# Optimization experiments

Measured on AMD Instinct MI355X. Metric: run time of the kernel, lower is better.

The kernel has to match this reference:

```python
import jax, jax.numpy as jnp
import numpy as np

EPS = 1e-4  # matches init_kwargs eps


def setup_inputs() -> dict:
    key = jax.random.key(0)
    k1, k2, k3 = jax.random.split(key, 3)
    B, C, T = 64, 256, 2048
    x = jax.random.normal(k1, (B, C, T), dtype=jnp.float32)
    # per-timestep BatchNorm affine params: [T, C]
    gamma = 1.0 + 0.1 * jax.random.normal(k2, (T, C), dtype=jnp.float32)
    beta = 0.01 * jax.random.normal(k3, (T, C), dtype=jnp.float32)
    return {"x": x, "gamma": gamma, "beta": beta}


def reference(x, gamma, beta):
    # BNTTv1 (training mode): every timestep's BatchNorm1d sees the FULL [B, C, T]
    # tensor, so the batch statistics (per-channel mean/var over B and T) are
    # identical across timesteps. Only the affine (gamma_t, beta_t) differs, and
    # the module keeps just slice t of layer t's output. Equivalent fused form:
    mean = jnp.mean(x, axis=(0, 2), keepdims=True)            # [1, C, 1]
    var = jnp.mean((x - mean) ** 2, axis=(0, 2), keepdims=True)  # biased var
    norm = (x - mean) * jax.lax.rsqrt(var + EPS)              # [B, C, T]
    # gamma/beta: [T, C] -> broadcast as [1, C, T]
    out = norm * gamma.T[None, :, :] + beta.T[None, :, :]
    return out
```

## Files before the change

kernel.cpp:

```cpp
#include <hip/hip_runtime.h>
#include <hip/hip_bf16.h>

#define B_ 64
#define C_ 256
#define T_ 2048
#define EPS_ 1e-4f
#define NPC ((float)(B_ * T_))

#define SPLITS 8
#define BPB (B_ / SPLITS)
#define T4 (T_ / 4)

typedef float f4 __attribute__((ext_vector_type(4)));

__global__ __launch_bounds__(256) void bntt_stats(const float* __restrict__ x,
                                                  float* __restrict__ partials) {
    const int c   = blockIdx.x & (C_ - 1);
    const int s   = blockIdx.x >> 8;
    const int tid = threadIdx.x;

    float sum = 0.0f, sumsq = 0.0f;
    const int b0 = s * BPB;
    #pragma unroll
    for (int b = 0; b < BPB; ++b) {
        const f4* p = (const f4*)(x + (size_t)(b0 + b) * (C_ * T_) + (size_t)c * T_);
        #pragma unroll
        for (int i = 0; i < T4 / 256; ++i) {
            f4 v = p[tid + i * 256];
            sum   += v.x + v.y + v.z + v.w;
            sumsq += v.x * v.x + v.y * v.y + v.z * v.z + v.w * v.w;
        }
    }
    #pragma unroll
    for (int off = 32; off > 0; off >>= 1) {
        sum   += __shfl_down(sum, off);
        sumsq += __shfl_down(sumsq, off);
    }
    __shared__ float ls[4], lss[4];
    const int wave = tid >> 6, lane = tid & 63;
    if (lane == 0) { ls[wave] = sum; lss[wave] = sumsq; }
    __syncthreads();
    if (tid == 0) {
        partials[s * C_ + c]                   = ls[0] + ls[1] + ls[2] + ls[3];
        partials[SPLITS * C_ + s * C_ + c]     = lss[0] + lss[1] + lss[2] + lss[3];
    }
}

__global__ __launch_bounds__(1024) void bntt_prep(const float* __restrict__ gamma,
                                                  const float* __restrict__ beta,
                                                  const float* __restrict__ partials,
                                                  float* __restrict__ scale,
                                                  float* __restrict__ shift) {
    __shared__ float tg[32][33];
    __shared__ float tb[32][33];
    __shared__ float smean[32], sistd[32];
    const int tx = threadIdx.x & 31;
    const int ty = threadIdx.x >> 5;
    const int c0 = blockIdx.x * 32;
    const int t0 = blockIdx.y * 32;

    if (threadIdx.x < 32) {
        const int c = c0 + threadIdx.x;
        float S = 0.0f, SS = 0.0f;
        #pragma unroll
        for (int s = 0; s < SPLITS; ++s) {
            S  += partials[s * C_ + c];
            SS += partials[SPLITS * C_ + s * C_ + c];
        }
        float mean = S / NPC;
        float var  = SS / NPC - mean * mean;
        smean[threadIdx.x] = mean;
        sistd[threadIdx.x] = rsqrtf(var + EPS_);
    }
    tg[ty][tx] = gamma[(size_t)(t0 + ty) * C_ + (c0 + tx)];
    tb[ty][tx] = beta [(size_t)(t0 + ty) * C_ + (c0 + tx)];
    __syncthreads();

    const float mean = smean[ty];
    const float istd = sistd[ty];
    const float sc = tg[tx][ty] * istd;
    scale[(size_t)(c0 + ty) * T_ + (t0 + tx)] = sc;
    shift[(size_t)(c0 + ty) * T_ + (t0 + tx)] = fmaf(-mean, sc, tb[tx][ty]);
}

#define BCHUNK 32
__global__ __launch_bounds__(256) void bntt_norm(const float* __restrict__ x,
                                                 const float* __restrict__ scale,
                                                 const float* __restrict__ shift,
                                                 float* __restrict__ out) {
    const int p   = (blockIdx.x & 511) * 256 + threadIdx.x;
    const int c   = p >> 9;
    const int t4  = p & (T4 - 1);
    const int b0  = (blockIdx.x >> 9) * BCHUNK;

    const f4 sc = ((const f4*)scale)[(size_t)c * T4 + t4];
    const f4 sh = ((const f4*)shift)[(size_t)c * T4 + t4];

    size_t idx = (size_t)(b0 * C_ + c) * T4 + t4;
    const size_t step = (size_t)C_ * T4;
    #pragma unroll 4
    for (int b = 0; b < BCHUNK; ++b) {
        f4 xv = ((const f4*)x)[idx];
        f4 o;
        o.x = fmaf(xv.x, sc.x, sh.x);
        o.y = fmaf(xv.y, sc.y, sh.y);
        o.z = fmaf(xv.z, sc.z, sh.z);
        o.w = fmaf(xv.w, sc.w, sh.w);
        __builtin_nontemporal_store(o, &((f4*)out)[idx]);
        idx += step;
    }
}

__global__ __launch_bounds__(256) void bntt_norm_fb(const float* __restrict__ x,
                                                    const float* __restrict__ gamma,
                                                    const float* __restrict__ beta,
                                                    const float* __restrict__ partials,
                                                    float* __restrict__ out) {
    const int p   = (blockIdx.x & 511) * 256 + threadIdx.x;
    const int c   = p >> 9;
    const int t4  = p & (T4 - 1);
    const int t   = t4 * 4;
    const int b0  = (blockIdx.x >> 9) * BCHUNK;

    float S = 0.0f, SS = 0.0f;
    #pragma unroll
    for (int s = 0; s < SPLITS; ++s) {
        S  += partials[s * C_ + c];
        SS += partials[SPLITS * C_ + s * C_ + c];
    }
    const float mean = S / NPC;
    const float istd = rsqrtf(SS / NPC - mean * mean + EPS_);

    f4 sc, sh;
    #pragma unroll
    for (int j = 0; j < 4; ++j) {
        float g  = gamma[(size_t)(t + j) * C_ + c];
        float bb = beta [(size_t)(t + j) * C_ + c];
        float s1 = g * istd;
        ((float*)&sc)[j] = s1;
        ((float*)&sh)[j] = fmaf(-mean, s1, bb);
    }
    size_t idx = (size_t)(b0 * C_ + c) * T4 + t4;
    const size_t step = (size_t)C_ * T4;
    #pragma unroll 4
    for (int b = 0; b < BCHUNK; ++b) {
        f4 xv = ((const f4*)x)[idx];
        f4 o;
        o.x = fmaf(xv.x, sc.x, sh.x);
        o.y = fmaf(xv.y, sc.y, sh.y);
        o.z = fmaf(xv.z, sc.z, sh.z);
        o.w = fmaf(xv.w, sc.w, sh.w);
        __builtin_nontemporal_store(o, &((f4*)out)[idx]);
        idx += step;
    }
}

extern "C" void kernel_launch(void* const* d_in, const int* in_sizes, int n_in,
                              void* d_out, int out_size, void* d_ws, size_t ws_size,
                              hipStream_t stream) {
    const float* x     = (const float*)d_in[0];
    const float* gamma = (const float*)d_in[1];
    const float* beta  = (const float*)d_in[2];
    float* out = (float*)d_out;

    float* partials = (float*)d_ws;
    float* scale    = partials + 2 * SPLITS * C_;
    float* shift    = scale + (size_t)C_ * T_;
    const size_t need = (2 * SPLITS * C_ + 2 * (size_t)C_ * T_) * sizeof(float);

    bntt_stats<<<C_ * SPLITS, 256, 0, stream>>>(x, partials);

    const int ngrid = (C_ * T4 / 256) * (B_ / BCHUNK);
    if (ws_size >= need) {
        dim3 pg(C_ / 32, T_ / 32);
        bntt_prep<<<pg, 1024, 0, stream>>>(gamma, beta, partials, scale, shift);
        bntt_norm<<<ngrid, 256, 0, stream>>>(x, scale, shift, out);
    } else {
        bntt_norm_fb<<<ngrid, 256, 0, stream>>>(x, gamma, beta, partials, out);
    }
}
```

Measured before the change: 253.5 us.

## Fuse stats, prep and normalize into one cooperative kernel with grid syncs

Replaces the three kernel launches (stats, scale/shift prep, normalize) with a single cooperative kernel of 1024 blocks that uses grid.sync between phases. Stats splits drop from 8 to 4 so that one block per channel-split covers the grid. The goal is to remove launch gaps and per-kernel tail effects between phases. The cost is two grid-wide barriers, and the kernel needs all 1024 blocks resident at once, with launch bounds set to 4 blocks per CU.

```diff
diff --git a/kernel.cpp b/kernel.cpp
--- a/kernel.cpp
+++ b/kernel.cpp
@@ -1,5 +1,7 @@
 #include <hip/hip_runtime.h>
-#include <hip/hip_bf16.h>
+#include <hip/hip_cooperative_groups.h>
+
+namespace cg = cooperative_groups;
 
 #define B_ 64
 #define C_ 256
@@ -7,11 +9,124 @@
 #define EPS_ 1e-4f
 #define NPC ((float)(B_ * T_))
 
-#define SPLITS 8
+#define T4 (T_ / 4)
+
+#define NBLK 1024
+#define SPLITS 4
 #define BPB (B_ / SPLITS)
-#define T4 (T_ / 4)
+#define BCHUNK 32
 
 typedef float f4 __attribute__((ext_vector_type(4)));
+
+__global__ __launch_bounds__(256, 4) void bntt_fused(const float* __restrict__ x,
+                                                     const float* __restrict__ gamma,
+                                                     const float* __restrict__ beta,
+                                                     float* __restrict__ out,
+                                                     float* __restrict__ ws) {
+    float* partials = ws;
+    float* scale    = ws + 2 * SPLITS * C_;
+    float* shift    = scale + (size_t)C_ * T_;
+
+    const int tid = threadIdx.x;
+    const int bid = blockIdx.x;
+    cg::grid_group grid = cg::this_grid();
+
+    {
+        const int c  = bid & (C_ - 1);
+        const int s  = bid >> 8;
+        const int b0 = s * BPB;
+        float sum = 0.0f, sumsq = 0.0f;
+        #pragma unroll 4
+        for (int b = 0; b < BPB; ++b) {
+            const f4* p = (const f4*)(x + (size_t)(b0 + b) * (C_ * T_) + (size_t)c * T_);
+            #pragma unroll
+            for (int i = 0; i < T4 / 256; ++i) {
+                f4 v = p[tid + i * 256];
+                sum   += v.x + v.y + v.z + v.w;
+                sumsq += v.x * v.x + v.y * v.y + v.z * v.z + v.w * v.w;
+            }
+        }
+        #pragma unroll
+        for (int off = 32; off > 0; off >>= 1) {
+            sum   += __shfl_down(sum, off);
+            sumsq += __shfl_down(sumsq, off);
+        }
+        __shared__ float ls[4], lss[4];
+        const int wave = tid >> 6, lane = tid & 63;
+        if (lane == 0) { ls[wave] = sum; lss[wave] = sumsq; }
+        __syncthreads();
+        if (tid == 0) {
+            partials[s * C_ + c]               = ls[0] + ls[1] + ls[2] + ls[3];
+            partials[SPLITS * C_ + s * C_ + c] = lss[0] + lss[1] + lss[2] + lss[3];
+        }
+    }
+    __threadfence();
+    grid.sync();
+
+    __shared__ float tg[32][33];
+    __shared__ float tb[32][33];
+    __shared__ float smean[32], sistd[32];
+    if (bid < 512) {
+        const int c0  = (bid & 7) * 32;
+        const int t0  = (bid >> 3) * 32;
+        const int tx  = tid & 31;
+        const int ty4 = tid >> 5;
+        if (tid < 32) {
+            const int c = c0 + tid;
+            float S = 0.0f, SS = 0.0f;
+            #pragma unroll
+            for (int s = 0; s < SPLITS; ++s) {
+                S  += partials[s * C_ + c];
+                SS += partials[SPLITS * C_ + s * C_ + c];
+            }
+            float mean = S / NPC;
+            smean[tid] = mean;
+            sistd[tid] = rsqrtf(SS / NPC - mean * mean + EPS_);
+        }
+        #pragma unroll
+        for (int r = 0; r < 4; ++r) {
+            const int ty = ty4 + r * 8;
+            tg[ty][tx] = gamma[(size_t)(t0 + ty) * C_ + (c0 + tx)];
+            tb[ty][tx] = beta [(size_t)(t0 + ty) * C_ + (c0 + tx)];
+        }
+        __syncthreads();
+        #pragma unroll
+        for (int r = 0; r < 4; ++r) {
+            const int ty  = ty4 + r * 8;
+            const float mean = smean[ty];
+            const float istd = sistd[ty];
+            const float sc = tg[tx][ty] * istd;
+            scale[(size_t)(c0 + ty) * T_ + (t0 + tx)] = sc;
+            shift[(size_t)(c0 + ty) * T_ + (t0 + tx)] = fmaf(-mean, sc, tb[tx][ty]);
+        }
+    }
+    __threadfence();
+    grid.sync();
+
+    {
+        const int p  = (bid & 511) * 256 + tid;
+        const int c  = p >> 9;
+        const int t4 = p & (T4 - 1);
+        const int b0 = (bid >> 9) * BCHUNK;
+
+        const f4 sc = ((const f4*)scale)[(size_t)c * T4 + t4];
+        const f4 sh = ((const f4*)shift)[(size_t)c * T4 + t4];
+
+        size_t idx = (size_t)(b0 * C_ + c) * T4 + t4;
+        const size_t step = (size_t)C_ * T4;
+        #pragma unroll 4
+        for (int b = 0; b < BCHUNK; ++b) {
+            f4 xv = ((const f4*)x)[idx];
+            f4 o;
+            o.x = fmaf(xv.x, sc.x, sh.x);
+            o.y = fmaf(xv.y, sc.y, sh.y);
+            o.z = fmaf(xv.z, sc.z, sh.z);
+            o.w = fmaf(xv.w, sc.w, sh.w);
+            __builtin_nontemporal_store(o, &((f4*)out)[idx]);
+            idx += step;
+        }
+    }
+}
 
 __global__ __launch_bounds__(256) void bntt_stats(const float* __restrict__ x,
                                                   float* __restrict__ partials) {
@@ -21,7 +136,7 @@
 
     float sum = 0.0f, sumsq = 0.0f;
     const int b0 = s * BPB;
-    #pragma unroll
+    #pragma unroll 4
     for (int b = 0; b < BPB; ++b) {
         const f4* p = (const f4*)(x + (size_t)(b0 + b) * (C_ * T_) + (size_t)c * T_);
         #pragma unroll
@@ -41,61 +156,40 @@
     if (lane == 0) { ls[wave] = sum; lss[wave] = sumsq; }
     __syncthreads();
     if (tid == 0) {
-        partials[s * C_ + c]                   = ls[0] + ls[1] + ls[2] + ls[3];
-        partials[SPLITS * C_ + s * C_ + c]     = lss[0] + lss[1] + lss[2] + lss[3];
-    }
-}
-
-__global__ __launch_bounds__(1024) void bntt_prep(const float* __restrict__ gamma,
-                                                  const float* __restrict__ beta,
-                                                  const float* __restrict__ partials,
-                                                  float* __restrict__ scale,
-                                                  float* __restrict__ shift) {
-    __shared__ float tg[32][33];
-    __shared__ float tb[32][33];
-    __shared__ float smean[32], sistd[32];
-    const int tx = threadIdx.x & 31;
-    const int ty = threadIdx.x >> 5;
-    const int c0 = blockIdx.x * 32;
-    const int t0 = blockIdx.y * 32;
-
-    if (threadIdx.x < 32) {
-        const int c = c0 + threadIdx.x;
-        float S = 0.0f, SS = 0.0f;
-        #pragma unroll
-        for (int s = 0; s < SPLITS; ++s) {
-            S  += partials[s * C_ + c];
-            SS += partials[SPLITS * C_ + s * C_ + c];
-        }
-        float mean = S / NPC;
-        float var  = SS / NPC - mean * mean;
-        smean[threadIdx.x] = mean;
-        sistd[threadIdx.x] = rsqrtf(var + EPS_);
-    }
-    tg[ty][tx] = gamma[(size_t)(t0 + ty) * C_ + (c0 + tx)];
-    tb[ty][tx] = beta [(size_t)(t0 + ty) * C_ + (c0 + tx)];
-    __syncthreads();
-
-    const float mean = smean[ty];
-    const float istd = sistd[ty];
-    const float sc = tg[tx][ty] * istd;
-    scale[(size_t)(c0 + ty) * T_ + (t0 + tx)] = sc;
-    shift[(size_t)(c0 + ty) * T_ + (t0 + tx)] = fmaf(-mean, sc, tb[tx][ty]);
-}
-
-#define BCHUNK 32
-__global__ __launch_bounds__(256) void bntt_norm(const float* __restrict__ x,
-                                                 const float* __restrict__ scale,
-                                                 const float* __restrict__ shift,
-                                                 float* __restrict__ out) {
+        partials[s * C_ + c]               = ls[0] + ls[1] + ls[2] + ls[3];
+        partials[SPLITS * C_ + s * C_ + c] = lss[0] + lss[1] + lss[2] + lss[3];
+    }
+}
+
+__global__ __launch_bounds__(256) void bntt_norm_fb(const float* __restrict__ x,
+                                                    const float* __restrict__ gamma,
+                                                    const float* __restrict__ beta,
+                                                    const float* __restrict__ partials,
+                                                    float* __restrict__ out) {
     const int p   = (blockIdx.x & 511) * 256 + threadIdx.x;
     const int c   = p >> 9;
     const int t4  = p & (T4 - 1);
+    const int t   = t4 * 4;
     const int b0  = (blockIdx.x >> 9) * BCHUNK;
 
-    const f4 sc = ((const f4*)scale)[(size_t)c * T4 + t4];
-    const f4 sh = ((const f4*)shift)[(size_t)c * T4 + t4];
-
+    float S = 0.0f, SS = 0.0f;
+    #pragma unroll
+    for (int s = 0; s < SPLITS; ++s) {
+        S  += partials[s * C_ + c];
+        SS += partials[SPLITS * C_ + s * C_ + c];
+    }
+    const float mean = S / NPC;
+    const float istd = rsqrtf(SS / NPC - mean * mean + EPS_);
+
+    f4 sc, sh;
+    #pragma unroll
+    for (int j = 0; j < 4; ++j) {
+        float g  = gamma[(size_t)(t + j) * C_ + c];
+        float bb = beta [(size_t)(t + j) * C_ + c];
+        float s1 = g * istd;
+        ((float*)&sc)[j] = s1;
+        ((float*)&sh)[j] = fmaf(-mean, s1, bb);
+    }
     size_t idx = (size_t)(b0 * C_ + c) * T4 + t4;
     const size_t step = (size_t)C_ * T4;
     #pragma unroll 4
@@ -111,50 +205,6 @@
     }
 }
 
-__global__ __launch_bounds__(256) void bntt_norm_fb(const float* __restrict__ x,
-                                                    const float* __restrict__ gamma,
-                                                    const float* __restrict__ beta,
-                                                    const float* __restrict__ partials,
-                                                    float* __restrict__ out) {
-    const int p   = (blockIdx.x & 511) * 256 + threadIdx.x;
-    const int c   = p >> 9;
-    const int t4  = p & (T4 - 1);
-    const int t   = t4 * 4;
-    const int b0  = (blockIdx.x >> 9) * BCHUNK;
-
-    float S = 0.0f, SS = 0.0f;
-    #pragma unroll
-    for (int s = 0; s < SPLITS; ++s) {
-        S  += partials[s * C_ + c];
-        SS += partials[SPLITS * C_ + s * C_ + c];
-    }
-    const float mean = S / NPC;
-    const float istd = rsqrtf(SS / NPC - mean * mean + EPS_);
-
-    f4 sc, sh;
-    #pragma unroll
-    for (int j = 0; j < 4; ++j) {
-        float g  = gamma[(size_t)(t + j) * C_ + c];
-        float bb = beta [(size_t)(t + j) * C_ + c];
-        float s1 = g * istd;
-        ((float*)&sc)[j] = s1;
-        ((float*)&sh)[j] = fmaf(-mean, s1, bb);
-    }
-    size_t idx = (size_t)(b0 * C_ + c) * T4 + t4;
-    const size_t step = (size_t)C_ * T4;
-    #pragma unroll 4
-    for (int b = 0; b < BCHUNK; ++b) {
-        f4 xv = ((const f4*)x)[idx];
-        f4 o;
-        o.x = fmaf(xv.x, sc.x, sh.x);
-        o.y = fmaf(xv.y, sc.y, sh.y);
-        o.z = fmaf(xv.z, sc.z, sh.z);
-        o.w = fmaf(xv.w, sc.w, sh.w);
-        __builtin_nontemporal_store(o, &((f4*)out)[idx]);
-        idx += step;
-    }
-}
-
 extern "C" void kernel_launch(void* const* d_in, const int* in_sizes, int n_in,
                               void* d_out, int out_size, void* d_ws, size_t ws_size,
                               hipStream_t stream) {
@@ -162,20 +212,17 @@
     const float* gamma = (const float*)d_in[1];
     const float* beta  = (const float*)d_in[2];
     float* out = (float*)d_out;
-
-    float* partials = (float*)d_ws;
-    float* scale    = partials + 2 * SPLITS * C_;
-    float* shift    = scale + (size_t)C_ * T_;
+    float* wsf = (float*)d_ws;
+
     const size_t need = (2 * SPLITS * C_ + 2 * (size_t)C_ * T_) * sizeof(float);
 
-    bntt_stats<<<C_ * SPLITS, 256, 0, stream>>>(x, partials);
-
-    const int ngrid = (C_ * T4 / 256) * (B_ / BCHUNK);
     if (ws_size >= need) {
-        dim3 pg(C_ / 32, T_ / 32);
-        bntt_prep<<<pg, 1024, 0, stream>>>(gamma, beta, partials, scale, shift);
-        bntt_norm<<<ngrid, 256, 0, stream>>>(x, scale, shift, out);
+        void* args[] = { (void*)&x, (void*)&gamma, (void*)&beta, (void*)&out, (void*)&wsf };
+        hipLaunchCooperativeKernel((void*)bntt_fused, dim3(NBLK), dim3(256),
+                                   args, 0, stream);
     } else {
-        bntt_norm_fb<<<ngrid, 256, 0, stream>>>(x, gamma, beta, partials, out);
-    }
-}
+        bntt_stats<<<C_ * SPLITS, 256, 0, stream>>>(x, wsf);
+        const int ngrid = (C_ * T4 / 256) * (B_ / BCHUNK);
+        bntt_norm_fb<<<ngrid, 256, 0, stream>>>(x, gamma, beta, wsf, out);
+    }
+}
```

New measurement: 698.2 us. +175.5%, slower.

## Fuse scale/shift prep into normalize kernel via shared-memory transpose of gamma/beta

Applied to the files above, without the earlier changes.

Removes the separate prep kernel that materialized transposed scale/shift arrays in workspace, and instead has each normalize block load a 64x16 gamma/beta tile into shared memory, transpose it, and compute per-thread scale and shift locally. Blocks are retiled to 16 channels by 16 float4 time positions so the transpose tile is small. This saves one kernel launch and the round trip of writing and re-reading 4 MB of scale/shift, at the cost of each batch-chunk block reloading gamma/beta and paying a syncthreads before streaming x. The uncoalesced fallback path is dropped.

```diff
diff --git a/kernel.cpp b/kernel.cpp
--- a/kernel.cpp
+++ b/kernel.cpp
@@ -1,5 +1,4 @@
 #include <hip/hip_runtime.h>
-#include <hip/hip_bf16.h>
 
 #define B_ 64
 #define C_ 256
@@ -10,6 +9,10 @@
 #define SPLITS 8
 #define BPB (B_ / SPLITS)
 #define T4 (T_ / 4)
+
+#define CTILE 16
+#define T4TILE 16
+#define BCHUNK 32
 
 typedef float f4 __attribute__((ext_vector_type(4)));
 
@@ -41,106 +44,67 @@
     if (lane == 0) { ls[wave] = sum; lss[wave] = sumsq; }
     __syncthreads();
     if (tid == 0) {
-        partials[s * C_ + c]                   = ls[0] + ls[1] + ls[2] + ls[3];
-        partials[SPLITS * C_ + s * C_ + c]     = lss[0] + lss[1] + lss[2] + lss[3];
+        partials[s * C_ + c]               = ls[0] + ls[1] + ls[2] + ls[3];
+        partials[SPLITS * C_ + s * C_ + c] = lss[0] + lss[1] + lss[2] + lss[3];
     }
 }
 
-__global__ __launch_bounds__(1024) void bntt_prep(const float* __restrict__ gamma,
-                                                  const float* __restrict__ beta,
-                                                  const float* __restrict__ partials,
-                                                  float* __restrict__ scale,
-                                                  float* __restrict__ shift) {
-    __shared__ float tg[32][33];
-    __shared__ float tb[32][33];
-    __shared__ float smean[32], sistd[32];
-    const int tx = threadIdx.x & 31;
-    const int ty = threadIdx.x >> 5;
-    const int c0 = blockIdx.x * 32;
-    const int t0 = blockIdx.y * 32;
+__global__ __launch_bounds__(256) void bntt_norm(const float* __restrict__ x,
+                                                 const float* __restrict__ gamma,
+                                                 const float* __restrict__ beta,
+                                                 const float* __restrict__ partials,
+                                                 float* __restrict__ out) {
+    __shared__ float sg[64][17];
+    __shared__ float sb[64][17];
+    __shared__ float smean[CTILE], sistd[CTILE];
 
-    if (threadIdx.x < 32) {
-        const int c = c0 + threadIdx.x;
+    const int tid    = threadIdx.x;
+    const int tile   = blockIdx.x & 511;
+    const int c0     = (tile >> 5) * CTILE;
+    const int t4base = (tile & 31) * T4TILE;
+    const int b0     = (blockIdx.x >> 9) * BCHUNK;
+
+    if (tid < CTILE) {
+        const int c = c0 + tid;
         float S = 0.0f, SS = 0.0f;
         #pragma unroll
         for (int s = 0; s < SPLITS; ++s) {
             S  += partials[s * C_ + c];
             SS += partials[SPLITS * C_ + s * C_ + c];
         }
-        float mean = S / NPC;
-        float var  = SS / NPC - mean * mean;
-        smean[threadIdx.x] = mean;
-        sistd[threadIdx.x] = rsqrtf(var + EPS_);
+        const float mean = S / NPC;
+        smean[tid] = mean;
+        sistd[tid] = rsqrtf(SS / NPC - mean * mean + EPS_);
     }
-    tg[ty][tx] = gamma[(size_t)(t0 + ty) * C_ + (c0 + tx)];
-    tb[ty][tx] = beta [(size_t)(t0 + ty) * C_ + (c0 + tx)];
+
+    {
+        const int cl = tid & 15;
+        const int tl0 = tid >> 4;
+        const int tbase = t4base * 4;
+        #pragma unroll
+        for (int it = 0; it < 4; ++it) {
+            const int tl = tl0 + it * 16;
+            const size_t gi = (size_t)(tbase + tl) * C_ + (c0 + cl);
+            sg[tl][cl] = gamma[gi];
+            sb[tl][cl] = beta[gi];
+        }
+    }
     __syncthreads();
 
-    const float mean = smean[ty];
-    const float istd = sistd[ty];
-    const float sc = tg[tx][ty] * istd;
-    scale[(size_t)(c0 + ty) * T_ + (t0 + tx)] = sc;
-    shift[(size_t)(c0 + ty) * T_ + (t0 + tx)] = fmaf(-mean, sc, tb[tx][ty]);
-}
-
-#define BCHUNK 32
-__global__ __launch_bounds__(256) void bntt_norm(const float* __restrict__ x,
-                                                 const float* __restrict__ scale,
-                                                 const float* __restrict__ shift,
-                                                 float* __restrict__ out) {
-    const int p   = (blockIdx.x & 511) * 256 + threadIdx.x;
-    const int c   = p >> 9;
-    const int t4  = p & (T4 - 1);
-    const int b0  = (blockIdx.x >> 9) * BCHUNK;
-
-    const f4 sc = ((const f4*)scale)[(size_t)c * T4 + t4];
-    const f4 sh = ((const f4*)shift)[(size_t)c * T4 + t4];
-
-    size_t idx = (size_t)(b0 * C_ + c) * T4 + t4;
-    const size_t step = (size_t)C_ * T4;
-    #pragma unroll 4
-    for (int b = 0; b < BCHUNK; ++b) {
-        f4 xv = ((const f4*)x)[idx];
-        f4 o;
-        o.x = fmaf(xv.x, sc.x, sh.x);
-        o.y = fmaf(xv.y, sc.y, sh.y);
-        o.z = fmaf(xv.z, sc.z, sh.z);
-        o.w = fmaf(xv.w, sc.w, sh.w);
-        __builtin_nontemporal_store(o, &((f4*)out)[idx]);
-        idx += step;
-    }
-}
-
-__global__ __launch_bounds__(256) void bntt_norm_fb(const float* __restrict__ x,
-                                                    const float* __restrict__ gamma,
-                                                    const float* __restrict__ beta,
-                                                    const float* __restrict__ partials,
-                                                    float* __restrict__ out) {
-    const int p   = (blockIdx.x & 511) * 256 + threadIdx.x;
-    const int c   = p >> 9;
-    const int t4  = p & (T4 - 1);
-    const int t   = t4 * 4;
-    const int b0  = (blockIdx.x >> 9) * BCHUNK;
-
-    float S = 0.0f, SS = 0.0f;
-    #pragma unroll
-    for (int s = 0; s < SPLITS; ++s) {
-        S  += partials[s * C_ + c];
-        SS += partials[SPLITS * C_ + s * C_ + c];
-    }
-    const float mean = S / NPC;
-    const float istd = rsqrtf(SS / NPC - mean * mean + EPS_);
-
+    const int t4i = tid & 15;
+    const int ci  = tid >> 4;
+    const float mean = smean[ci];
+    const float istd = sistd[ci];
     f4 sc, sh;
     #pragma unroll
     for (int j = 0; j < 4; ++j) {
-        float g  = gamma[(size_t)(t + j) * C_ + c];
-        float bb = beta [(size_t)(t + j) * C_ + c];
-        float s1 = g * istd;
+        const int tl = t4i * 4 + j;
+        const float s1 = sg[tl][ci] * istd;
         ((float*)&sc)[j] = s1;
-        ((float*)&sh)[j] = fmaf(-mean, s1, bb);
+        ((float*)&sh)[j] = fmaf(-mean, s1, sb[tl][ci]);
     }
-    size_t idx = (size_t)(b0 * C_ + c) * T4 + t4;
+
+    size_t idx = ((size_t)b0 * C_ + (c0 + ci)) * T4 + (t4base + t4i);
     const size_t step = (size_t)C_ * T4;
     #pragma unroll 4
     for (int b = 0; b < BCHUNK; ++b) {
@@ -162,20 +126,10 @@
     const float* gamma = (const float*)d_in[1];
     const float* beta  = (const float*)d_in[2];
     float* out = (float*)d_out;
-
     float* partials = (float*)d_ws;
-    float* scale    = partials + 2 * SPLITS * C_;
-    float* shift    = scale + (size_t)C_ * T_;
-    const size_t need = (2 * SPLITS * C_ + 2 * (size_t)C_ * T_) * sizeof(float);
 
     bntt_stats<<<C_ * SPLITS, 256, 0, stream>>>(x, partials);
 
-    const int ngrid = (C_ * T4 / 256) * (B_ / BCHUNK);
-    if (ws_size >= need) {
-        dim3 pg(C_ / 32, T_ / 32);
-        bntt_prep<<<pg, 1024, 0, stream>>>(gamma, beta, partials, scale, shift);
-        bntt_norm<<<ngrid, 256, 0, stream>>>(x, scale, shift, out);
-    } else {
-        bntt_norm_fb<<<ngrid, 256, 0, stream>>>(x, gamma, beta, partials, out);
-    }
+    const int ngrid = (C_ / CTILE) * (T4 / T4TILE) * (B_ / BCHUNK);
+    bntt_norm<<<ngrid, 256, 0, stream>>>(x, gamma, beta, partials, out);
 }
```

Result: no change. 251.6 us (-0.8%).
